# Performance work log

Measured on AMD Instinct MI355X. Metric: run time of the kernel, lower is better.

The kernel has to match this reference:

```python
import jax, jax.numpy as jnp
import numpy as np

B, S, D, H = 2, 2048, 1024, 16
DK = D // H
LARGE = 1e9
LN_EPS = 1e-5


def sinusoidal_embeddings(seq_len, d):
    pos = jnp.arange(seq_len, dtype=jnp.float32)[:, None]          # [S,1]
    i = jnp.arange(d // 2, dtype=jnp.float32)[None, :]             # [1,d/2]
    freq = jnp.exp(-(2.0 * i / d) * jnp.log(10000.0))
    ang = pos * freq                                               # [S,d/2]
    pe = jnp.zeros((seq_len, d), dtype=jnp.float32)
    pe = pe.at[:, 0::2].set(jnp.sin(ang))
    pe = pe.at[:, 1::2].set(jnp.cos(ang))
    return pe


def setup_inputs() -> dict:
    key = jax.random.key(0)
    ks = jax.random.split(key, 6)
    sc = 1.0 / np.sqrt(D)
    return {
        "X": jax.random.normal(ks[0], (B, S, D), jnp.float32),
        "W_q": jax.random.normal(ks[1], (D, D), jnp.float32) * sc,
        "W_k": jax.random.normal(ks[2], (D, D), jnp.float32) * sc,
        "W_v": jax.random.normal(ks[3], (D, D), jnp.float32) * sc,
        "W_o": jax.random.normal(ks[4], (D, D), jnp.float32) * sc,
        "alpha": jnp.ones((1, H, S - 1, 1), jnp.float32),
        "ln_scale": jnp.ones((D,), jnp.float32),
        "ln_bias": jnp.zeros((D,), jnp.float32),
    }


def reference(X, W_q, W_k, W_v, W_o, alpha, ln_scale, ln_bias):
    # projections (torch Linear: x @ W.T), split heads -> [B,H,S,dk]
    def proj(W):
        return jnp.einsum('bsd,ed->bse', X, W).reshape(B, S, H, DK).transpose(0, 2, 1, 3)
    Q, K, V = proj(W_q), proj(W_k), proj(W_v)

    # EMA smear on K along sequence
    a = jax.nn.sigmoid(alpha)                                      # [1,H,S-1,1]
    smeared = K[:, :, 1:, :] * a + K[:, :, :-1, :] * (1.0 - a)
    K = jnp.concatenate([K[:, :, 0:1, :], smeared], axis=2)

    # inline sinusoidal positional embeddings added to K and Q
    pe = sinusoidal_embeddings(S, DK)                              # [S,dk]
    K = K + pe
    Q = Q + pe

    mask = jnp.triu(jnp.ones((S, S), jnp.float32), k=1) * (-LARGE)
    scores = jnp.einsum('bhqd,bhkd->bhqk', Q, K) / jnp.sqrt(jnp.float32(DK)) + mask
    weights = jax.nn.softmax(scores, axis=-1)
    attn = jnp.einsum('bhqk,bhkd->bhqd', weights, V)               # [B,H,S,dk]
    attn = attn.transpose(0, 2, 1, 3).reshape(B, S, D)

    Y = jnp.einsum('bsd,ed->bse', attn, W_o) + X

    # LayerNorm
    mu = jnp.mean(Y, axis=-1, keepdims=True)
    var = jnp.mean(jnp.square(Y - mu), axis=-1, keepdims=True)
    Y = (Y - mu) / jnp.sqrt(var + LN_EPS) * ln_scale + ln_bias
    return Y
```

## Files before the change

kernel.cpp:

```cpp
#include <hip/hip_runtime.h>


#define LB __launch_bounds__(256)

typedef unsigned short u16;
typedef unsigned int u32;
typedef __attribute__((ext_vector_type(2))) unsigned int u32x2;
typedef __attribute__((ext_vector_type(4))) unsigned short us4;
typedef __attribute__((ext_vector_type(8))) unsigned short us8;
typedef __attribute__((ext_vector_type(8))) __bf16 bf8;
typedef __attribute__((ext_vector_type(4))) float f4;
typedef __attribute__((ext_vector_type(4))) short s4;

#define QSCALE 0.18033688011112042f

#if __has_builtin(__builtin_amdgcn_exp2f)
#define EXP2 __builtin_amdgcn_exp2f
#else
#define EXP2 exp2f
#endif

static __device__ __forceinline__ float bf2f(u16 h) {
  union { unsigned int u; float f; } c; c.u = ((unsigned int)h) << 16; return c.f;
}
static __device__ __forceinline__ u16 f2bf(float f) {
  union { float f; unsigned int u; } c; c.f = f;
  unsigned int u = c.u + 0x7FFFu + ((c.u >> 16) & 1u);
  return (u16)(u >> 16);
}
#if __has_builtin(__builtin_amdgcn_cvt_pk_bf16_f32)
typedef __attribute__((ext_vector_type(2))) __bf16 bf2v;
static __device__ __forceinline__ us4 pk_bf16x4(f4 v) {
  bf2v lo = __builtin_amdgcn_cvt_pk_bf16_f32(v[0], v[1]);
  bf2v hi = __builtin_amdgcn_cvt_pk_bf16_f32(v[2], v[3]);
  u32x2 r = {__builtin_bit_cast(u32, lo), __builtin_bit_cast(u32, hi)};
  return __builtin_bit_cast(us4, r);
}
#else
static __device__ __forceinline__ us4 pk_bf16x4(f4 v) {
  return us4{f2bf(v[0]), f2bf(v[1]), f2bf(v[2]), f2bf(v[3])};
}
#endif
static __device__ __forceinline__ float pe_val(int s, int dk) {
  float fr = __expf((float)(dk & ~1) * (-9.210340371976184f / 64.0f));
  float ang = (float)s * fr;
  return (dk & 1) ? __cosf(ang) : __sinf(ang);
}

#if __has_builtin(__builtin_amdgcn_mfma_f32_16x16x16bf16_1k)
static __device__ __forceinline__ f4 mfma16(us4 a, us4 b, f4 c) {
  return __builtin_amdgcn_mfma_f32_16x16x16bf16_1k(
      __builtin_bit_cast(s4, a), __builtin_bit_cast(s4, b), c, 0, 0, 0);
}
#elif __has_builtin(__builtin_amdgcn_mfma_f32_16x16x16_bf16)
typedef __attribute__((ext_vector_type(4))) __bf16 bf4;
static __device__ __forceinline__ f4 mfma16(us4 a, us4 b, f4 c) {
  return __builtin_amdgcn_mfma_f32_16x16x16_bf16(
      __builtin_bit_cast(bf4, a), __builtin_bit_cast(bf4, b), c, 0, 0, 0);
}
#else
static __device__ __forceinline__ f4 mfma16(us4 a, us4 b, f4 c) {
  asm volatile("v_mfma_f32_16x16x16_bf16 %0, %1, %2, %0" : "+v"(c) : "v"(a), "v"(b));
  return c;
}
#endif

#define GLDS(gp, lp) __builtin_amdgcn_global_load_lds( \
    (const __attribute__((address_space(1))) void*)(gp), \
    (__attribute__((address_space(3))) void*)(lp), 16, 0, 0)

__global__ LB void cvt_kernel(const float* __restrict__ X, const float* __restrict__ Wq,
                              const float* __restrict__ Wk, const float* __restrict__ Wv,
                              const float* __restrict__ Wo, u16* __restrict__ Xb,
                              u16* __restrict__ Wcat, u16* __restrict__ Wob) {
  const unsigned t = blockIdx.x * 256 + threadIdx.x;
  const float* src; u16* dst; size_t off;
  if (t < (512u << 10))      { src = X;  dst = Xb;                off = t; }
  else if (t < (640u << 10)) { src = Wq; dst = Wcat;              off = t - (512u << 10); }
  else if (t < (768u << 10)) { src = Wk; dst = Wcat + (1u << 20); off = t - (640u << 10); }
  else if (t < (896u << 10)) { src = Wv; dst = Wcat + (2u << 20); off = t - (768u << 10); }
  else                       { src = Wo; dst = Wob;               off = t - (896u << 10); }
  off *= 8;
  f4 a = *(const f4*)(src + off);
  f4 b = *(const f4*)(src + off + 4);
  us8 o = {f2bf(a[0]), f2bf(a[1]), f2bf(a[2]), f2bf(a[3]),
           f2bf(b[0]), f2bf(b[1]), f2bf(b[2]), f2bf(b[3])};
  *(us8*)(dst + off) = o;
}

static __device__ __forceinline__ void gemm_core(
    const u16* __restrict__ Abase, const u16* __restrict__ Bbase,
    u16* Als, u16* Bls, int m0, int n0, int tid, f4 acc[4][4]) {
  const int w = tid >> 6, lane = tid & 63;
  const int l16 = lane & 15, quad = lane >> 4;
  const int wm = w & 1, wn = w >> 1;
  for (int kk = 0; kk < 1024; kk += 32) {
    __syncthreads();
#pragma unroll
    for (int it = 0; it < 2; it++) {
      int cb = (w * 2 + it) * 64;
      int c = cb + lane;
      int row = c >> 2, kc = c & 3;
      GLDS(Abase + (size_t)(m0 + row) * 1024 + kk + kc * 8, &Als[cb * 8]);
      GLDS(Bbase + (size_t)(n0 + row) * 1024 + kk + kc * 8, &Bls[cb * 8]);
    }
    __syncthreads();
    bf8 af[4], bfr[4];
#pragma unroll
    for (int mt = 0; mt < 4; mt++)
      af[mt] = __builtin_bit_cast(bf8, *(const us8*)(&Als[(wm * 64 + mt * 16 + l16) * 32 + quad * 8]));
#pragma unroll
    for (int nt = 0; nt < 4; nt++)
      bfr[nt] = __builtin_bit_cast(bf8, *(const us8*)(&Bls[(wn * 64 + nt * 16 + l16) * 32 + quad * 8]));
#pragma unroll
    for (int mt = 0; mt < 4; mt++)
#pragma unroll
      for (int nt = 0; nt < 4; nt++)
        acc[mt][nt] = __builtin_amdgcn_mfma_f32_16x16x32_bf16(af[mt], bfr[nt], acc[mt][nt], 0, 0, 0);
  }
}

__global__ LB void gemm_qkv(const u16* __restrict__ Xb, const u16* __restrict__ Wcat,
                            u16* __restrict__ Qb, u16* __restrict__ Kraw,
                            u16* __restrict__ Vp) {
  __shared__ u16 Als[128 * 32];
  __shared__ u16 Bls[128 * 32];
  const int tid = threadIdx.x;
  const int m0 = blockIdx.y * 128, n0 = blockIdx.x * 128;
  f4 acc[4][4];
#pragma unroll
  for (int a = 0; a < 4; a++)
#pragma unroll
    for (int b = 0; b < 4; b++) acc[a][b] = f4{0.f, 0.f, 0.f, 0.f};
  gemm_core(Xb, Wcat, Als, Bls, m0, n0, tid, acc);

  const int w = tid >> 6, lane = tid & 63;
  const int l16 = lane & 15, quad = lane >> 4;
  const int wm = w & 1, wn = w >> 1;
  const int z = blockIdx.x >> 3;
#pragma unroll
  for (int mt = 0; mt < 4; mt++)
#pragma unroll
    for (int nt = 0; nt < 4; nt++)
#pragma unroll
      for (int r = 0; r < 4; r++) {
        int m = m0 + wm * 64 + mt * 16 + quad * 4 + r;
        int nn = (n0 + wn * 64 + nt * 16 + l16) & 1023;
        float v = acc[mt][nt][r];
        int b = m >> 11, s = m & 2047, h = nn >> 6, dk = nn & 63;
        size_t bhoff = (size_t)(b * 16 + h) * (2048 * 64);
        if (z == 0) {
          Qb[bhoff + (size_t)s * 64 + dk] = f2bf((v + pe_val(s, dk)) * QSCALE);
        } else if (z == 1) {
          Kraw[bhoff + (size_t)s * 64 + dk] = f2bf(v);
        } else {
          int kb = s >> 6, sl = s & 63;
          int t = sl >> 4, Qq = (sl >> 2) & 3, jj = sl & 3;
          int dn = dk >> 4, lv = dk & 15;
          Vp[bhoff + (size_t)kb * 4096 + ((t * 4 + dn) * 64 + Qq * 16 + lv) * 4 + jj] = f2bf(v);
        }
      }
}

__global__ LB void ema_pe(const u16* __restrict__ Kraw, const float* __restrict__ alpha,
                          u16* __restrict__ Kp) {
  int idx = blockIdx.x * 256 + threadIdx.x;
  int b8  = idx & 7;
  int s   = (idx >> 3) & 2047;
  int bh  = idx >> 14;
  int dk8 = b8 * 8;
  size_t base = ((size_t)bh * 2048 + s) * 64 + dk8;
  us8 kc = *(const us8*)(Kraw + base);
  float kv[8];
#pragma unroll
  for (int j = 0; j < 8; j++) kv[j] = bf2f(kc[j]);
  if (s > 0) {
    us8 kp = *(const us8*)(Kraw + base - 64);
    float aa = alpha[(bh & 15) * 2047 + s - 1];
    float a = 1.0f / (1.0f + __expf(-aa));
#pragma unroll
    for (int j = 0; j < 8; j++) kv[j] = kv[j] * a + bf2f(kp[j]) * (1.0f - a);
  }
  us8 o;
#pragma unroll
  for (int j = 0; j < 8; j++) o[j] = f2bf(kv[j] + pe_val(s, dk8 + j));
  int kt16 = s >> 4, c = b8 >> 2, quad = b8 & 3, l16s = s & 15;
  size_t off = (size_t)bh * (2048 * 64) + (size_t)kt16 * 1024 + (c * 64 + quad * 16 + l16s) * 8;
  *(us8*)(Kp + off) = o;
}

template<bool MASK>
static __device__ __forceinline__ void attn_step(
    int kb, const u16* __restrict__ Kt, const u16* __restrict__ Vt,
    const bf8* qf, f4* acc, float& lsum, int lane, int quad, int qrel0) {
  const u16* kbase = Kt + (size_t)kb * 4096;
  const u16* vbase = Vt + (size_t)kb * 4096;
  f4 sc[4];
#pragma unroll
  for (int t = 0; t < 4; t++) sc[t] = f4{0.f, 0.f, 0.f, 0.f};
#pragma unroll
  for (int t = 0; t < 4; t++)
#pragma unroll
    for (int c = 0; c < 2; c++) {
      bf8 kf = __builtin_bit_cast(bf8, *(const us8*)(kbase + (t * 2 + c) * 512 + lane * 8));
      sc[t] = __builtin_amdgcn_mfma_f32_16x16x32_bf16(kf, qf[c], sc[t], 0, 0, 0);
    }
  us4 pf[4];
#pragma unroll
  for (int t = 0; t < 4; t++) {
    f4 pv;
#pragma unroll
    for (int r = 0; r < 4; r++) {
      float s = sc[t][r];
      if (MASK && (t * 16 + quad * 4 + r > qrel0)) s = -1e30f;
      float p = EXP2(s);
      lsum += p;
      pv[r] = p;
    }
    pf[t] = pk_bf16x4(pv);
  }
#pragma unroll
  for (int t = 0; t < 4; t++)
#pragma unroll
    for (int dn = 0; dn < 4; dn++) {
      us4 vf = *(const us4*)(vbase + ((t * 4 + dn) * 64 + lane) * 4);
      acc[dn] = mfma16(vf, pf[t], acc[dn]);
    }
}

__global__ LB void attn_kernel(const u16* __restrict__ Qb, const u16* __restrict__ Kp,
                               const u16* __restrict__ Vp, u16* __restrict__ Ab) {
  __shared__ float comb[2][64][20];
  const int tid = threadIdx.x, w = tid >> 6, lane = tid & 63;
  const int l16 = lane & 15, quad = lane >> 4;
  const int idx = blockIdx.x;
  const int bh = idx & 31;
  const int qg = 63 - (idx >> 5);
  const int qt = w & 1;
  const int h2 = w >> 1;
  const int qw = qg * 32 + qt * 16;
  const size_t bhoff = (size_t)bh * (2048 * 64);
  const u16* Kt = Kp + bhoff;
  const u16* Vt = Vp + bhoff;

  bf8 qf[2];
#pragma unroll
  for (int c = 0; c < 2; c++)
    qf[c] = __builtin_bit_cast(bf8, *(const us8*)(Qb + bhoff + (size_t)(qw + l16) * 64 + c * 32 + quad * 8));

  f4 acc[4];
#pragma unroll
  for (int dn = 0; dn < 4; dn++) acc[dn] = f4{0.f, 0.f, 0.f, 0.f};
  float lsum = 0.f;

  const int T  = (qw >> 6) + 1;
  const int Th = (T + 1) >> 1;
  const int kbs = h2 ? Th : 0;
  const int kbe = h2 ? T : Th;
  const int e_un = (kbe < T - 1) ? kbe : (T - 1);
  for (int kb = kbs; kb < e_un; kb++)
    attn_step<false>(kb, Kt, Vt, qf, acc, lsum, lane, quad, 0);
  if (kbe == T && kbe > kbs)
    attn_step<true>(T - 1, Kt, Vt, qf, acc, lsum, lane, quad, qw + l16 - (T - 1) * 64);

  if (h2) {
    float* d = &comb[qt][lane][0];
    *(f4*)(d)      = acc[0];
    *(f4*)(d + 4)  = acc[1];
    *(f4*)(d + 8)  = acc[2];
    *(f4*)(d + 12) = acc[3];
    d[16] = lsum;
  }
  __syncthreads();
  if (!h2) {
    const float* s = &comb[qt][lane][0];
    acc[0] += *(const f4*)(s);
    acc[1] += *(const f4*)(s + 4);
    acc[2] += *(const f4*)(s + 8);
    acc[3] += *(const f4*)(s + 12);
    lsum += s[16];
    lsum += __shfl_xor(lsum, 16, 64);
    lsum += __shfl_xor(lsum, 32, 64);
    float rinv = 1.0f / lsum;
    const int b = bh >> 4, h = bh & 15;
    const int q = qw + l16;
    u16* orow = Ab + ((size_t)(b * 2048 + q)) * 1024 + h * 64;
#pragma unroll
    for (int dn = 0; dn < 4; dn++) {
      us4 o = pk_bf16x4(f4{acc[dn][0] * rinv, acc[dn][1] * rinv,
                           acc[dn][2] * rinv, acc[dn][3] * rinv});
      *(us4*)(orow + dn * 16 + quad * 4) = o;
    }
  }
}

__global__ LB void gemm_out(const u16* __restrict__ Ab, const u16* __restrict__ Wob,
                            const float* __restrict__ X, float* __restrict__ Yp) {
  __shared__ u16 Als[128 * 32];
  __shared__ u16 Bls[128 * 32];
  const int tid = threadIdx.x;
  const int m0 = blockIdx.y * 128, n0 = blockIdx.x * 128;
  f4 acc[4][4];
#pragma unroll
  for (int a = 0; a < 4; a++)
#pragma unroll
    for (int b = 0; b < 4; b++) acc[a][b] = f4{0.f, 0.f, 0.f, 0.f};
  gemm_core(Ab, Wob, Als, Bls, m0, n0, tid, acc);

  const int w = tid >> 6, lane = tid & 63;
  const int l16 = lane & 15, quad = lane >> 4;
  const int wm = w & 1, wn = w >> 1;
#pragma unroll
  for (int mt = 0; mt < 4; mt++)
#pragma unroll
    for (int nt = 0; nt < 4; nt++)
#pragma unroll
      for (int r = 0; r < 4; r++) {
        int m = m0 + wm * 64 + mt * 16 + quad * 4 + r;
        int n = n0 + wn * 64 + nt * 16 + l16;
        size_t o = (size_t)m * 1024 + n;
        Yp[o] = acc[mt][nt][r] + X[o];
      }
}

__global__ LB void ln_kernel(const float* __restrict__ Y, const float* __restrict__ g,
                             const float* __restrict__ bta, float* __restrict__ out) {
  __shared__ float ls[4], lsq[4];
  const int row = blockIdx.x, tid = threadIdx.x;
  const int w = tid >> 6, lane = tid & 63;
  f4 v = *(const f4*)(Y + (size_t)row * 1024 + tid * 4);
  float s  = v[0] + v[1] + v[2] + v[3];
  float sq = v[0] * v[0] + v[1] * v[1] + v[2] * v[2] + v[3] * v[3];
#pragma unroll
  for (int d = 1; d < 64; d <<= 1) { s += __shfl_xor(s, d, 64); sq += __shfl_xor(sq, d, 64); }
  if (lane == 0) { ls[w] = s; lsq[w] = sq; }
  __syncthreads();
  s  = ls[0] + ls[1] + ls[2] + ls[3];
  sq = lsq[0] + lsq[1] + lsq[2] + lsq[3];
  float mu  = s * (1.0f / 1024.0f);
  float var = sq * (1.0f / 1024.0f) - mu * mu;
  float rs  = rsqrtf(var + 1e-5f);
  f4 o;
#pragma unroll
  for (int j = 0; j < 4; j++) {
    int col = tid * 4 + j;
    o[j] = (v[j] - mu) * rs * g[col] + bta[col];
  }
  *(f4*)(out + (size_t)row * 1024 + tid * 4) = o;
}

extern "C" void kernel_launch(void* const* d_in, const int* in_sizes, int n_in,
                              void* d_out, int out_size, void* d_ws, size_t ws_size,
                              hipStream_t stream) {
  (void)in_sizes; (void)n_in; (void)out_size; (void)ws_size;
  const float* X  = (const float*)d_in[0];
  const float* Wq = (const float*)d_in[1];
  const float* Wk = (const float*)d_in[2];
  const float* Wv = (const float*)d_in[3];
  const float* Wo = (const float*)d_in[4];
  const float* al = (const float*)d_in[5];
  const float* g  = (const float*)d_in[6];
  const float* bt = (const float*)d_in[7];

  char* ws = (char*)d_ws;
  float* Yp   = (float*)(ws);
  u16*   Xb   = (u16*)(ws + ((size_t)16 << 20));
  u16*   Wcat = (u16*)(ws + ((size_t)24 << 20));
  u16*   Wob  = (u16*)(ws + ((size_t)30 << 20));
  u16*   Qb   = (u16*)(ws + ((size_t)32 << 20));
  u16*   Kraw = (u16*)(ws + ((size_t)40 << 20));
  u16*   Ab   = (u16*)(ws + ((size_t)40 << 20));
  u16*   Kp   = (u16*)(ws + ((size_t)48 << 20));
  u16*   Vp   = (u16*)(ws + ((size_t)56 << 20));

  cvt_kernel<<<dim3(4096), 256, 0, stream>>>(X, Wq, Wk, Wv, Wo, Xb, Wcat, Wob);
  gemm_qkv<<<dim3(24, 32), 256, 0, stream>>>(Xb, Wcat, Qb, Kraw, Vp);
  ema_pe<<<dim3(2048), 256, 0, stream>>>(Kraw, al, Kp);
  attn_kernel<<<dim3(2048), 256, 0, stream>>>(Qb, Kp, Vp, Ab);
  gemm_out<<<dim3(8, 32), 256, 0, stream>>>(Ab, Wob, X, Yp);
  ln_kernel<<<dim3(4096), 256, 0, stream>>>(Yp, g, bt, (float*)d_out);
}
```

Measured before the change: 211.9 us.

## Stage K/V tiles in LDS with double buffering and pair causal query blocks

The attention kernel now has each block handle 64 query rows, one 16-row strip per wave, over two phases that pair a long and a short causal query group to balance work. K and V tiles are loaded once per block into double-buffered LDS through direct global-to-LDS loads and shared by all four waves, where before each wave read them separately from global memory. The two-wave key split with its LDS reduction is removed, and the grid shrinks from 2048 to 512 blocks. This adds a barrier per key tile and lowers the block count, which may reduce parallelism and latency hiding on the GPU.

```diff
diff --git a/kernel.cpp b/kernel.cpp
--- a/kernel.cpp
+++ b/kernel.cpp
@@ -190,11 +190,9 @@
 }
 
 template<bool MASK>
-static __device__ __forceinline__ void attn_step(
-    int kb, const u16* __restrict__ Kt, const u16* __restrict__ Vt,
+static __device__ __forceinline__ void attn_step_lds(
+    const u16* kbase, const u16* vbase,
     const bf8* qf, f4* acc, float& lsum, int lane, int quad, int qrel0) {
-  const u16* kbase = Kt + (size_t)kb * 4096;
-  const u16* vbase = Vt + (size_t)kb * 4096;
   f4 sc[4];
 #pragma unroll
   for (int t = 0; t < 4; t++) sc[t] = f4{0.f, 0.f, 0.f, 0.f};
@@ -230,59 +228,67 @@
 
 __global__ LB void attn_kernel(const u16* __restrict__ Qb, const u16* __restrict__ Kp,
                                const u16* __restrict__ Vp, u16* __restrict__ Ab) {
-  __shared__ float comb[2][64][20];
+  __shared__ u16 Kls[2][4096];
+  __shared__ u16 Vls[2][4096];
   const int tid = threadIdx.x, w = tid >> 6, lane = tid & 63;
   const int l16 = lane & 15, quad = lane >> 4;
   const int idx = blockIdx.x;
   const int bh = idx & 31;
-  const int qg = 63 - (idx >> 5);
-  const int qt = w & 1;
-  const int h2 = w >> 1;
-  const int qw = qg * 32 + qt * 16;
+  const int p  = idx >> 5;
   const size_t bhoff = (size_t)bh * (2048 * 64);
   const u16* Kt = Kp + bhoff;
   const u16* Vt = Vp + bhoff;
-
-  bf8 qf[2];
-#pragma unroll
-  for (int c = 0; c < 2; c++)
-    qf[c] = __builtin_bit_cast(bf8, *(const us8*)(Qb + bhoff + (size_t)(qw + l16) * 64 + c * 32 + quad * 8));
-
-  f4 acc[4];
-#pragma unroll
-  for (int dn = 0; dn < 4; dn++) acc[dn] = f4{0.f, 0.f, 0.f, 0.f};
-  float lsum = 0.f;
-
-  const int T  = (qw >> 6) + 1;
-  const int Th = (T + 1) >> 1;
-  const int kbs = h2 ? Th : 0;
-  const int kbe = h2 ? T : Th;
-  const int e_un = (kbe < T - 1) ? kbe : (T - 1);
-  for (int kb = kbs; kb < e_un; kb++)
-    attn_step<false>(kb, Kt, Vt, qf, acc, lsum, lane, quad, 0);
-  if (kbe == T && kbe > kbs)
-    attn_step<true>(T - 1, Kt, Vt, qf, acc, lsum, lane, quad, qw + l16 - (T - 1) * 64);
-
-  if (h2) {
-    float* d = &comb[qt][lane][0];
-    *(f4*)(d)      = acc[0];
-    *(f4*)(d + 4)  = acc[1];
-    *(f4*)(d + 8)  = acc[2];
-    *(f4*)(d + 12) = acc[3];
-    d[16] = lsum;
-  }
-  __syncthreads();
-  if (!h2) {
-    const float* s = &comb[qt][lane][0];
-    acc[0] += *(const f4*)(s);
-    acc[1] += *(const f4*)(s + 4);
-    acc[2] += *(const f4*)(s + 8);
-    acc[3] += *(const f4*)(s + 12);
-    lsum += s[16];
+  const int b = bh >> 4, h = bh & 15;
+
+  for (int ph = 0; ph < 2; ph++) {
+    const int g = ph ? p : 31 - p;
+    const int T = g + 1;
+    const int qw = g * 64 + w * 16;
+
+    bf8 qf[2];
+#pragma unroll
+    for (int c = 0; c < 2; c++)
+      qf[c] = __builtin_bit_cast(bf8, *(const us8*)(Qb + bhoff + (size_t)(qw + l16) * 64 + c * 32 + quad * 8));
+
+    f4 acc[4];
+#pragma unroll
+    for (int dn = 0; dn < 4; dn++) acc[dn] = f4{0.f, 0.f, 0.f, 0.f};
+    float lsum = 0.f;
+
+    {
+      const u16* kg = Kt + w * 1024;
+      const u16* vg = Vt + w * 1024;
+      GLDS(kg + lane * 8,       &Kls[0][w * 1024]);
+      GLDS(kg + 512 + lane * 8, &Kls[0][w * 1024 + 512]);
+      GLDS(vg + lane * 8,       &Vls[0][w * 1024]);
+      GLDS(vg + 512 + lane * 8, &Vls[0][w * 1024 + 512]);
+    }
+    asm volatile("s_waitcnt vmcnt(0)" ::: "memory");
+    __builtin_amdgcn_s_barrier();
+
+    for (int kb = 0; kb < T; kb++) {
+      const int cur = kb & 1;
+      if (kb + 1 < T) {
+        const u16* kg = Kt + (size_t)(kb + 1) * 4096 + w * 1024;
+        const u16* vg = Vt + (size_t)(kb + 1) * 4096 + w * 1024;
+        u16* kl = &Kls[cur ^ 1][w * 1024];
+        u16* vl = &Vls[cur ^ 1][w * 1024];
+        GLDS(kg + lane * 8, kl);
+        GLDS(kg + 512 + lane * 8, kl + 512);
+        GLDS(vg + lane * 8, vl);
+        GLDS(vg + 512 + lane * 8, vl + 512);
+      }
+      if (kb == T - 1)
+        attn_step_lds<true>(&Kls[cur][0], &Vls[cur][0], qf, acc, lsum, lane, quad, w * 16 + l16);
+      else
+        attn_step_lds<false>(&Kls[cur][0], &Vls[cur][0], qf, acc, lsum, lane, quad, 0);
+      asm volatile("s_waitcnt vmcnt(0)" ::: "memory");
+      __builtin_amdgcn_s_barrier();
+    }
+
     lsum += __shfl_xor(lsum, 16, 64);
     lsum += __shfl_xor(lsum, 32, 64);
     float rinv = 1.0f / lsum;
-    const int b = bh >> 4, h = bh & 15;
     const int q = qw + l16;
     u16* orow = Ab + ((size_t)(b * 2048 + q)) * 1024 + h * 64;
 #pragma unroll
@@ -376,7 +382,7 @@
   cvt_kernel<<<dim3(4096), 256, 0, stream>>>(X, Wq, Wk, Wv, Wo, Xb, Wcat, Wob);
   gemm_qkv<<<dim3(24, 32), 256, 0, stream>>>(Xb, Wcat, Qb, Kraw, Vp);
   ema_pe<<<dim3(2048), 256, 0, stream>>>(Kraw, al, Kp);
-  attn_kernel<<<dim3(2048), 256, 0, stream>>>(Qb, Kp, Vp, Ab);
+  attn_kernel<<<dim3(512), 256, 0, stream>>>(Qb, Kp, Vp, Ab);
   gemm_out<<<dim3(8, 32), 256, 0, stream>>>(Ab, Wob, X, Yp);
   ln_kernel<<<dim3(4096), 256, 0, stream>>>(Yp, g, bt, (float*)d_out);
 }
```

Measured after the change: 193.5 us. 1.09x faster.
